# Kernel tuning notes

Hardware: AMD Instinct MI355X
Metric: run time of the kernel (lower is better)

Reference implementation:

```python
import jax, jax.numpy as jnp
import numpy as np

B, N, C = 8, 1024, 768
NH, HD = 12, 64  # num_heads, head_dim
S = 32           # spatial_size (H = W = S, N = S*S)


def _rel_pos_idx(h, w):
    # Standard Swin-style relative position index, shape (h*w, h*w)
    coords = np.stack(np.meshgrid(np.arange(h), np.arange(w), indexing='ij'))  # (2, h, w)
    coords = coords.reshape(2, -1)                                             # (2, N)
    rel = coords[:, :, None] - coords[:, None, :]                              # (2, N, N)
    rel = rel.transpose(1, 2, 0).astype(np.int64)                              # (N, N, 2)
    rel[:, :, 0] += h - 1
    rel[:, :, 1] += w - 1
    rel[:, :, 0] *= 2 * w - 1
    return rel.sum(-1).astype(np.int32)                                        # (N, N)


def setup_inputs() -> dict:
    key = jax.random.key(0)
    ks = jax.random.split(key, 7)
    lim = (1.0 / C) ** 0.5
    x = jax.random.normal(ks[0], (B, N, C), dtype=jnp.float32)
    Wq = jax.random.uniform(ks[1], (C, C), minval=-lim, maxval=lim, dtype=jnp.float32)
    bq = jax.random.uniform(ks[2], (C,), minval=-lim, maxval=lim, dtype=jnp.float32)
    Wkv = jax.random.uniform(ks[3], (2 * C, C), minval=-lim, maxval=lim, dtype=jnp.float32)
    bkv = jax.random.uniform(ks[4], (2 * C,), minval=-lim, maxval=lim, dtype=jnp.float32)
    rel_bias = jax.random.uniform(ks[5], ((2 * S - 1) * (2 * S - 1), NH), dtype=jnp.float32)
    rel_idx = jnp.asarray(_rel_pos_idx(S, S))  # (N, N) int32
    return {"x": x, "Wq": Wq, "bq": bq, "Wkv": Wkv, "bkv": bkv,
            "rel_bias": rel_bias, "rel_idx": rel_idx, "H": S, "W": S}


def reference(x, Wq, bq, Wkv, bkv, rel_bias, rel_idx, H, W):
    b, n, c = x.shape
    scale = HD ** (-0.5)
    # Q projection: (B, NH, N, HD)
    q = (x @ Wq.T + bq).reshape(b, n, NH, HD).transpose(0, 2, 1, 3) * scale
    # KV projection (reduction_factor == 1, no downsample)
    kv = (x @ Wkv.T + bkv).reshape(b, n, 2, NH, HD)
    k = kv[:, :, 0].transpose(0, 2, 1, 3)  # (B, NH, N, HD)
    v = kv[:, :, 1].transpose(0, 2, 1, 3)  # (B, NH, N, HD)
    # Attention scores + gathered relative-position bias
    attn = jnp.einsum('bhqd,bhkd->bhqk', q, k)
    bias = rel_bias[rel_idx]                # (N, N, NH) gather
    attn = attn + bias.transpose(2, 0, 1)[None]
    attn = jax.nn.softmax(attn, axis=-1)
    out = jnp.einsum('bhqk,bhkd->bhqd', attn, v)
    out = out.transpose(0, 2, 1, 3).reshape(b, n, c)
    # NOTE: original forward never applies self.proj; dropout p=0 is identity.
    return out
```

## Files before the change

### kernel.cpp

```cpp
#include <hip/hip_runtime.h>


using bf16x8 = __attribute__((ext_vector_type(8))) short;
using f32x4  = __attribute__((ext_vector_type(4))) float;
using f32x16 = __attribute__((ext_vector_type(16))) float;
using s16x4  = __attribute__((ext_vector_type(4))) short;
using f32x4v = __attribute__((ext_vector_type(4))) float;

#define DEVINL __device__ __forceinline__

#if __has_builtin(__builtin_amdgcn_exp2f)
#define EXP2(x) __builtin_amdgcn_exp2f(x)
#else
#define EXP2(x) __expf((x) * 0.6931471805599453f)
#endif

DEVINL float b2f(short s) {
  union { unsigned u; float f; } v;
  v.u = ((unsigned)(unsigned short)s) << 16;
  return v.f;
}
DEVINL short f2b(float f) {
  union { float f; unsigned u; } v; v.f = f;
  unsigned r = v.u + 0x7fffu + ((v.u >> 16) & 1u);
  return (short)(r >> 16);
}

DEVINL unsigned cvtpk(float lo, float hi) {
  unsigned r;
  asm("v_cvt_pk_bf16_f32 %0, %1, %2" : "=v"(r) : "v"(lo), "v"(hi));
  return r;
}
DEVINL void plswap(unsigned& a, unsigned& b) {
  asm("v_permlane32_swap_b32 %0, %1" : "+v"(a), "+v"(b));
}

DEVINL int is_bf16(const unsigned* xraw) {
  int cnt = 0;
#pragma unroll
  for (int i = 0; i < 64; ++i) {
    unsigned e = (xraw[i] >> 7) & 0xffu;
    cnt += (e >= 0x60u && e <= 0xa0u) ? 1 : 0;
  }
  return cnt >= 48;
}

DEVINL void gl_lds16(const short* g, short* l) {
  __builtin_amdgcn_global_load_lds(
      (const __attribute__((address_space(1))) unsigned int*)g,
      (__attribute__((address_space(3))) unsigned int*)l, 16, 0, 0);
}

__global__ __launch_bounds__(256) void convert_kernel(
    const void* __restrict__ x, const void* __restrict__ wq,
    const void* __restrict__ bq, const void* __restrict__ wkv,
    const void* __restrict__ bkv, const void* __restrict__ rb,
    short* __restrict__ xc, short* __restrict__ wqc, short* __restrict__ bqc,
    short* __restrict__ wkvc, short* __restrict__ bkvc,
    short* __restrict__ rbc) {
  const int bf = is_bf16((const unsigned*)x);
  long t = ((long)blockIdx.x * 256 + threadIdx.x) * 4;
  const void* src; short* dst; long i;
  if (t < 6291456L)      { src = x;   dst = xc;   i = t; }
  else if (t < 6881280L) { src = wq;  dst = wqc;  i = t - 6291456L; }
  else if (t < 6882048L) { src = bq;  dst = bqc;  i = t - 6881280L; }
  else if (t < 8061696L) { src = wkv; dst = wkvc; i = t - 6882048L; }
  else if (t < 8063232L) { src = bkv; dst = bkvc; i = t - 8061696L; }
  else if (t < 8110860L) { src = rb;  dst = rbc;  i = t - 8063232L; }
  else return;
  s16x4 o;
  if (bf) {
    o = *(const s16x4*)((const short*)src + i);
  } else {
    f32x4v v = *(const f32x4v*)((const float*)src + i);
    o[0] = f2b(v[0]); o[1] = f2b(v[1]); o[2] = f2b(v[2]); o[3] = f2b(v[3]);
  }
  *(s16x4*)(dst + i) = o;
}

__global__ __launch_bounds__(256) void bias_pack_kernel(
    const int* __restrict__ rel_idx, const short* __restrict__ rel_bias,
    short* __restrict__ bias_pk) {
  int t = blockIdx.x * 256 + threadIdx.x;
  int hi = t & 1, q = (t >> 1) & 1023, kt2 = t >> 11;
  union { unsigned long long u[3]; short s[12]; } row[16];
#pragma unroll
  for (int r = 0; r < 16; ++r) {
    int k = kt2 * 32 + (r & 3) + 8 * (r >> 2) + 4 * hi;
    int idx = rel_idx[q * 1024 + k];
    const unsigned long long* src =
        (const unsigned long long*)(rel_bias + (size_t)idx * 12);
    row[r].u[0] = src[0]; row[r].u[1] = src[1]; row[r].u[2] = src[2];
  }
#pragma unroll
  for (int hh = 0; hh < 12; ++hh) {
    union { short s[16]; bf16x8 v[2]; } o;
#pragma unroll
    for (int r = 0; r < 16; ++r)
      o.s[r] = f2b(b2f(row[r].s[hh]) * 1.44269504f);
    short* dst = bias_pk + ((((size_t)hh * 32 + kt2) * 1024 + q) * 2 + hi) * 16;
    *(bf16x8*)dst = o.v[0];
    *(bf16x8*)(dst + 8) = o.v[1];
  }
}

__global__ __launch_bounds__(512, 6) void qkv_gemm_kernel(
    const short* __restrict__ x, const short* __restrict__ wq,
    const short* __restrict__ wkv, const short* __restrict__ bq,
    const short* __restrict__ bkv, short* __restrict__ qbuf,
    short* __restrict__ kbuf, short* __restrict__ vtbuf) {
  __shared__ short lds_a[8192];
  __shared__ short lds_b[8192];
  const int tid = threadIdx.x;
  const int w = tid >> 6, lane = tid & 63, quad = lane >> 4, l15 = lane & 15;
  const int bid = blockIdx.x;
  const int xcd = bid & 7, local = bid >> 3;
  const int m_tile = xcd * 8 + (local & 7), n_tile = local >> 3;
  const int m0 = m_tile * 128, n0 = n_tile * 128;
  const short* wsrc = (n0 < 768) ? (wq + (size_t)n0 * 768)
                                 : (wkv + (size_t)(n0 - 768) * 768);
  const int wm = (w & 1) * 64, wn = (w >> 1) * 32;
  const int lrow = lane >> 3;
  const int lcol = ((lane & 7) ^ lrow) * 8;
  f32x4 acc[4][2] = {};

  for (int k0 = 0; k0 < 768; k0 += 64) {
    __syncthreads();
#pragma unroll
    for (int c = 0; c < 2; ++c) {
      int r0 = (c * 8 + w) * 8;
      gl_lds16(x + (size_t)(m0 + r0 + lrow) * 768 + k0 + lcol, &lds_a[r0 * 64]);
      gl_lds16(wsrc + (size_t)(r0 + lrow) * 768 + k0 + lcol, &lds_b[r0 * 64]);
    }
    __syncthreads();
#pragma unroll
    for (int ks = 0; ks < 2; ++ks) {
      bf16x8 af[4], bg[2];
#pragma unroll
      for (int i = 0; i < 4; ++i) {
        int row = wm + i * 16 + l15;
        af[i] = *(const bf16x8*)
            &lds_a[row * 64 + (((ks * 4 + quad) ^ (row & 7)) * 8)];
      }
#pragma unroll
      for (int j = 0; j < 2; ++j) {
        int row = wn + j * 16 + l15;
        bg[j] = *(const bf16x8*)
            &lds_b[row * 64 + (((ks * 4 + quad) ^ (row & 7)) * 8)];
      }
#pragma unroll
      for (int i = 0; i < 4; ++i)
#pragma unroll
        for (int j = 0; j < 2; ++j)
          acc[i][j] = __builtin_amdgcn_mfma_f32_16x16x32_bf16(af[i], bg[j],
                                                              acc[i][j], 0, 0, 0);
    }
  }

  float biasv[2];
#pragma unroll
  for (int j = 0; j < 2; ++j) {
    int ncol = n0 + wn + j * 16 + l15;
    biasv[j] = b2f(ncol < 768 ? bq[ncol] : bkv[ncol - 768]);
  }
#pragma unroll
  for (int i = 0; i < 4; ++i)
#pragma unroll
    for (int r = 0; r < 4; ++r) {
      int m = m0 + wm + i * 16 + quad * 4 + r;
      int bb = m >> 10, nrow = m & 1023;
#pragma unroll
      for (int j = 0; j < 2; ++j) {
        int ncol = n0 + wn + j * 16 + l15;
        float v = acc[i][j][r] + biasv[j];
        if (n0 < 768) {
          int hh = ncol >> 6, d = ncol & 63;
          qbuf[(((size_t)bb * 12 + hh) * 1024 + nrow) * 64 + d] =
              f2b(v * 0.18033688f);
        } else if (n0 < 1536) {
          int c2 = ncol - 768, hh = c2 >> 6, d = c2 & 63;
          kbuf[(((size_t)bb * 12 + hh) * 1024 + nrow) * 64 + d] = f2b(v);
        } else {
          int c2 = ncol - 1536, hh = c2 >> 6, d = c2 & 63;
          vtbuf[(((size_t)bb * 12 + hh) * 64 + d) * 1024 + nrow] = f2b(v);
        }
      }
    }
}

__global__ __launch_bounds__(256, 3) void attn_kernel(
    const short* __restrict__ qbuf, const short* __restrict__ kbuf,
    const short* __restrict__ vtbuf, const short* __restrict__ bias_pk,
    const void* __restrict__ xraw, void* __restrict__ out) {
  __shared__ short lds_k[64 * 64];
  __shared__ short lds_v[64 * 64];
  const int tid = threadIdx.x;
  const int w = tid >> 6, lane = tid & 63, l31 = lane & 31, hi = lane >> 5;
  const int qt = blockIdx.y, bh = blockIdx.x;
  const int b = bh / 12, h = bh - b * 12;
  const short* kbase = kbuf + (size_t)bh * 65536;
  const short* vbase = vtbuf + (size_t)bh * 65536;
  const int q0 = qt * 128 + w * 32;

  bf16x8 qf[4];
#pragma unroll
  for (int ds = 0; ds < 4; ++ds)
    qf[ds] = *(const bf16x8*)(qbuf +
        ((size_t)(bh * 1024 + q0 + l31) * 64 + ds * 16 + hi * 8));

  bf16x8 ones;
#pragma unroll
  for (int z = 0; z < 8; ++z) ones[z] = (short)0x3F80;

  f32x16 acc_o[2] = {};
  f32x16 acc_l = {};

  const int srow = tid >> 3, sc = tid & 7;

  bf16x8 rk[2], rv[2];
#pragma unroll
  for (int p = 0; p < 2; ++p) {
    int rr = p * 32 + srow;
    rk[p] = *(const bf16x8*)(kbase + (size_t)rr * 64 + sc * 8);
    rv[p] = *(const bf16x8*)(vbase + (size_t)rr * 1024 + sc * 8);
  }

  const short* bias_base =
      bias_pk + (((size_t)h * 32 * 1024 + q0 + l31) * 2 + hi) * 16;

  for (int kt = 0; kt < 16; ++kt) {
    __syncthreads();
#pragma unroll
    for (int p = 0; p < 2; ++p) {
      int rr = p * 32 + srow;
      int wa = rr * 64 + ((sc ^ (rr & 7)) * 8);
      *(bf16x8*)&lds_k[wa] = rk[p];
      *(bf16x8*)&lds_v[wa] = rv[p];
    }
    __syncthreads();
    if (kt < 15) {
#pragma unroll
      for (int p = 0; p < 2; ++p) {
        int rr = p * 32 + srow;
        rk[p] = *(const bf16x8*)(kbase +
                  (size_t)((kt + 1) * 64 + rr) * 64 + sc * 8);
        rv[p] = *(const bf16x8*)(vbase +
                  (size_t)rr * 1024 + (kt + 1) * 64 + sc * 8);
      }
    }

#pragma unroll
    for (int st = 0; st < 2; ++st) {
      const short* bb = bias_base + (size_t)(kt * 2 + st) * (1024 * 2 * 16);
      bf16x8 bv0 = *(const bf16x8*)bb;
      bf16x8 bv1 = *(const bf16x8*)(bb + 8);
      f32x16 s;
#pragma unroll
      for (int r = 0; r < 8; ++r) s[r] = b2f(bv0[r]);
#pragma unroll
      for (int r = 0; r < 8; ++r) s[8 + r] = b2f(bv1[r]);
#pragma unroll
      for (int ds = 0; ds < 4; ++ds) {
        int krow = st * 32 + l31;
        bf16x8 kf = *(const bf16x8*)
            &lds_k[krow * 64 + (((ds * 2 + hi) ^ (krow & 7)) * 8)];
        s = __builtin_amdgcn_mfma_f32_32x32x16_bf16(kf, qf[ds], s, 0, 0, 0);
      }
      float p[16];
#pragma unroll
      for (int r = 0; r < 16; ++r) p[r] = EXP2(s[r]);
#pragma unroll
      for (int kk = 0; kk < 2; ++kk) {
        unsigned wa = cvtpk(p[kk * 8 + 0], p[kk * 8 + 1]);
        unsigned wb = cvtpk(p[kk * 8 + 4], p[kk * 8 + 5]);
        unsigned wc = cvtpk(p[kk * 8 + 2], p[kk * 8 + 3]);
        unsigned wd = cvtpk(p[kk * 8 + 6], p[kk * 8 + 7]);
        plswap(wa, wb);
        plswap(wc, wd);
        union { unsigned u[4]; bf16x8 v; } pa;
        pa.u[0] = wa; pa.u[1] = wc; pa.u[2] = wb; pa.u[3] = wd;
        acc_l = __builtin_amdgcn_mfma_f32_32x32x16_bf16(pa.v, ones, acc_l,
                                                        0, 0, 0);
#pragma unroll
        for (int dt = 0; dt < 2; ++dt) {
          int vd = dt * 32 + l31;
          bf16x8 vf = *(const bf16x8*)
              &lds_v[vd * 64 + (((st * 4 + kk * 2 + hi) ^ (vd & 7)) * 8)];
          acc_o[dt] = __builtin_amdgcn_mfma_f32_32x32x16_bf16(pa.v, vf,
                                                              acc_o[dt],
                                                              0, 0, 0);
        }
      }
    }
  }

  const int bfo = is_bf16((const unsigned*)xraw);
  short* outb = (short*)out;
  float* outf = (float*)out;
  if (bfo) {
#pragma unroll
    for (int r = 0; r < 16; ++r) {
      float inv = 1.0f / fmaxf(acc_l[r], 1e-35f);
      int q = qt * 128 + w * 32 + (r & 3) + 8 * (r >> 2) + 4 * hi;
      size_t o0 = ((size_t)b * 1024 + q) * 768 + h * 64 + l31;
      outb[o0] = f2b(acc_o[0][r] * inv);
      outb[o0 + 32] = f2b(acc_o[1][r] * inv);
    }
  } else {
#pragma unroll
    for (int r = 0; r < 16; ++r) {
      float inv = 1.0f / fmaxf(acc_l[r], 1e-35f);
      int q = qt * 128 + w * 32 + (r & 3) + 8 * (r >> 2) + 4 * hi;
      size_t o0 = ((size_t)b * 1024 + q) * 768 + h * 64 + l31;
      outf[o0] = acc_o[0][r] * inv;
      outf[o0 + 32] = acc_o[1][r] * inv;
    }
  }
}

extern "C" void kernel_launch(void* const* d_in, const int* in_sizes, int n_in,
                              void* d_out, int out_size, void* d_ws, size_t ws_size,
                              hipStream_t stream) {
  const void* x        = d_in[0];
  const void* wq       = d_in[1];
  const void* bq       = d_in[2];
  const void* wkv      = d_in[3];
  const void* bkv      = d_in[4];
  const void* rel_bias = d_in[5];
  const int*  rel_idx  = (const int*)d_in[6];

  char* ws = (char*)d_ws;
  short* qbuf    = (short*)(ws);
  short* kbuf    = (short*)(ws + 12582912);
  short* vtbuf   = (short*)(ws + 25165824);
  short* bias_pk = (short*)(ws + 37748736);
  short* xc      = (short*)(ws + 62914560);
  short* wqc     = (short*)(ws + 75497472);
  short* bqc     = (short*)(ws + 76677120);
  short* wkvc    = (short*)(ws + 76678656);
  short* bkvc    = (short*)(ws + 79037952);
  short* rbc     = (short*)(ws + 79041024);

  convert_kernel<<<7921, 256, 0, stream>>>(x, wq, bq, wkv, bkv, rel_bias,
                                           xc, wqc, bqc, wkvc, bkvc, rbc);
  bias_pack_kernel<<<256, 256, 0, stream>>>(rel_idx, rbc, bias_pk);
  qkv_gemm_kernel<<<1152, 512, 0, stream>>>(xc, wqc, wkvc, bqc, bkvc,
                                            qbuf, kbuf, vtbuf);
  attn_kernel<<<dim3(96, 8), 256, 0, stream>>>(qbuf, kbuf, vtbuf, bias_pk,
                                               x, (void*)d_out);
}
```

Measured before the change: 199.0 us.

## Double-buffer QKV GEMM with 256x128 tiles and prefetch two k-steps ahead

The QKV projection GEMM moves from 128x128 tiles with a single LDS buffer and two barriers per k-step to 256x128 tiles. It uses a two-stage LDS ring that prefetches the next k-tile while MFMAs run, with manual vmcnt waits and s_setprio around the MFMA block. Each wave now computes a 64x64 sub-tile for more reuse per LDS fragment load. This is meant to hide global-to-LDS latency and cut barrier overhead. In exchange the grid halves to 576 blocks with lower occupancy (launch bounds 2) and uses more LDS and registers.

```diff
diff --git a/kernel.cpp b/kernel.cpp
--- a/kernel.cpp
+++ b/kernel.cpp
@@ -104,62 +104,83 @@
   }
 }
 
-__global__ __launch_bounds__(512, 6) void qkv_gemm_kernel(
+__global__ __launch_bounds__(512, 2) void qkv_gemm_kernel(
     const short* __restrict__ x, const short* __restrict__ wq,
     const short* __restrict__ wkv, const short* __restrict__ bq,
     const short* __restrict__ bkv, short* __restrict__ qbuf,
     short* __restrict__ kbuf, short* __restrict__ vtbuf) {
-  __shared__ short lds_a[8192];
-  __shared__ short lds_b[8192];
+  __shared__ short lds[2][24576];
   const int tid = threadIdx.x;
   const int w = tid >> 6, lane = tid & 63, quad = lane >> 4, l15 = lane & 15;
   const int bid = blockIdx.x;
   const int xcd = bid & 7, local = bid >> 3;
-  const int m_tile = xcd * 8 + (local & 7), n_tile = local >> 3;
-  const int m0 = m_tile * 128, n0 = n_tile * 128;
+  const int m_tile = xcd * 4 + (local & 3), n_tile = local >> 2;
+  const int m0 = m_tile * 256, n0 = n_tile * 128;
   const short* wsrc = (n0 < 768) ? (wq + (size_t)n0 * 768)
                                  : (wkv + (size_t)(n0 - 768) * 768);
-  const int wm = (w & 1) * 64, wn = (w >> 1) * 32;
+  const int wm = (w >> 1) * 64, wn = (w & 1) * 64;
   const int lrow = lane >> 3;
   const int lcol = ((lane & 7) ^ lrow) * 8;
-  f32x4 acc[4][2] = {};
-
-  for (int k0 = 0; k0 < 768; k0 += 64) {
-    __syncthreads();
+  f32x4 acc[4][4] = {};
+
+  auto STAGE = [&](short* bp, int k0) {
+#pragma unroll
+    for (int c = 0; c < 4; ++c) {
+      int r0 = (c * 8 + w) * 8;
+      gl_lds16(x + (size_t)(m0 + r0 + lrow) * 768 + k0 + lcol, bp + r0 * 64);
+    }
 #pragma unroll
     for (int c = 0; c < 2; ++c) {
       int r0 = (c * 8 + w) * 8;
-      gl_lds16(x + (size_t)(m0 + r0 + lrow) * 768 + k0 + lcol, &lds_a[r0 * 64]);
-      gl_lds16(wsrc + (size_t)(r0 + lrow) * 768 + k0 + lcol, &lds_b[r0 * 64]);
-    }
-    __syncthreads();
+      gl_lds16(wsrc + (size_t)(r0 + lrow) * 768 + k0 + lcol,
+               bp + 16384 + r0 * 64);
+    }
+  };
+
+  STAGE(lds[0], 0);
+  STAGE(lds[1], 64);
+  asm volatile("s_waitcnt vmcnt(6)\n\ts_barrier" ::: "memory");
+
+#pragma unroll 2
+  for (int kt = 0; kt < 12; ++kt) {
+    short* cur = lds[kt & 1];
 #pragma unroll
     for (int ks = 0; ks < 2; ++ks) {
-      bf16x8 af[4], bg[2];
+      bf16x8 af[4], bg[4];
 #pragma unroll
       for (int i = 0; i < 4; ++i) {
         int row = wm + i * 16 + l15;
         af[i] = *(const bf16x8*)
-            &lds_a[row * 64 + (((ks * 4 + quad) ^ (row & 7)) * 8)];
-      }
-#pragma unroll
-      for (int j = 0; j < 2; ++j) {
+            &cur[row * 64 + (((ks * 4 + quad) ^ (row & 7)) * 8)];
+      }
+#pragma unroll
+      for (int j = 0; j < 4; ++j) {
         int row = wn + j * 16 + l15;
         bg[j] = *(const bf16x8*)
-            &lds_b[row * 64 + (((ks * 4 + quad) ^ (row & 7)) * 8)];
-      }
+            &cur[16384 + row * 64 + (((ks * 4 + quad) ^ (row & 7)) * 8)];
+      }
+      __builtin_amdgcn_s_setprio(1);
 #pragma unroll
       for (int i = 0; i < 4; ++i)
 #pragma unroll
-        for (int j = 0; j < 2; ++j)
+        for (int j = 0; j < 4; ++j)
           acc[i][j] = __builtin_amdgcn_mfma_f32_16x16x32_bf16(af[i], bg[j],
-                                                              acc[i][j], 0, 0, 0);
-    }
-  }
-
-  float biasv[2];
-#pragma unroll
-  for (int j = 0; j < 2; ++j) {
+                                                              acc[i][j],
+                                                              0, 0, 0);
+      __builtin_amdgcn_s_setprio(0);
+    }
+    asm volatile("s_barrier" ::: "memory");
+    if (kt + 2 < 12) {
+      STAGE(cur, (kt + 2) * 64);
+      asm volatile("s_waitcnt vmcnt(6)\n\ts_barrier" ::: "memory");
+    } else {
+      asm volatile("s_waitcnt vmcnt(0)\n\ts_barrier" ::: "memory");
+    }
+  }
+
+  float biasv[4];
+#pragma unroll
+  for (int j = 0; j < 4; ++j) {
     int ncol = n0 + wn + j * 16 + l15;
     biasv[j] = b2f(ncol < 768 ? bq[ncol] : bkv[ncol - 768]);
   }
@@ -170,7 +191,7 @@
       int m = m0 + wm + i * 16 + quad * 4 + r;
       int bb = m >> 10, nrow = m & 1023;
 #pragma unroll
-      for (int j = 0; j < 2; ++j) {
+      for (int j = 0; j < 4; ++j) {
         int ncol = n0 + wn + j * 16 + l15;
         float v = acc[i][j][r] + biasv[j];
         if (n0 < 768) {
@@ -344,8 +365,8 @@
   convert_kernel<<<7921, 256, 0, stream>>>(x, wq, bq, wkv, bkv, rel_bias,
                                            xc, wqc, bqc, wkvc, bkvc, rbc);
   bias_pack_kernel<<<256, 256, 0, stream>>>(rel_idx, rbc, bias_pk);
-  qkv_gemm_kernel<<<1152, 512, 0, stream>>>(xc, wqc, wkvc, bqc, bkvc,
-                                            qbuf, kbuf, vtbuf);
+  qkv_gemm_kernel<<<576, 512, 0, stream>>>(xc, wqc, wkvc, bqc, bkvc,
+                                           qbuf, kbuf, vtbuf);
   attn_kernel<<<dim3(96, 8), 256, 0, stream>>>(qbuf, kbuf, vtbuf, bias_pk,
                                                x, (void*)d_out);
 }
```

Result: slower. 216.5 us (+8.8%).
